# Optimization experiments

Hardware: AMD Instinct MI355X
Metric: run time of the kernel (lower is better)

Reference implementation:

```python
import jax, jax.numpy as jnp
import numpy as np

N_NODES = 100000
N_EDGES = 640000
C_IN = 128
C_OUT = 128
E_DIM = 64
LN_EPS = 1e-5


def setup_inputs() -> dict:
    key = jax.random.key(0)
    ks = jax.random.split(key, 10)
    x = jax.random.normal(ks[0], (N_NODES, C_IN), dtype=jnp.float32)
    edge_index = jax.random.randint(ks[1], (2, N_EDGES), 0, N_NODES, dtype=jnp.int32)
    edge_attr = jax.random.normal(ks[2], (N_EDGES, E_DIM), dtype=jnp.float32)
    # lin_edge: edge_dim -> in_channels
    We = jax.random.normal(ks[3], (E_DIM, C_IN), dtype=jnp.float32) / np.sqrt(E_DIM)
    be = jnp.zeros((C_IN,), dtype=jnp.float32)
    # mlp: Linear(C, 2C) -> LayerNorm(2C) -> ReLU -> Linear(2C, C_OUT)
    W1 = jax.random.normal(ks[4], (C_IN, 2 * C_IN), dtype=jnp.float32) / np.sqrt(C_IN)
    b1 = jnp.zeros((2 * C_IN,), dtype=jnp.float32)
    gamma = jnp.ones((2 * C_IN,), dtype=jnp.float32)
    beta = jnp.zeros((2 * C_IN,), dtype=jnp.float32)
    W2 = jax.random.normal(ks[5], (2 * C_IN, C_OUT), dtype=jnp.float32) / np.sqrt(2 * C_IN)
    b2 = jnp.zeros((C_OUT,), dtype=jnp.float32)
    eps = jnp.zeros((1,), dtype=jnp.float32)  # learnable GIN epsilon, init 0
    return {"x": x, "edge_index": edge_index, "edge_attr": edge_attr,
            "We": We, "be": be, "W1": W1, "b1": b1, "gamma": gamma,
            "beta": beta, "W2": W2, "b2": b2, "eps": eps}


def reference(x, edge_index, edge_attr, We, be, W1, b1, gamma, beta, W2, b2, eps):
    # edge feature projection: [E, E_DIM] @ [E_DIM, C] -> [E, C]
    real_edge_attr = edge_attr @ We + be
    # gather source-node features (edge_index[1]), add edge features, relu
    message = jax.nn.relu(x[edge_index[1]] + real_edge_attr)  # [E, C]
    # scatter-add to destination nodes (edge_index[0])
    message_reduce = jax.ops.segment_sum(message, edge_index[0], num_segments=x.shape[0])
    h = (1.0 + eps) * x + message_reduce  # [N, C]
    # MLP: Linear -> LayerNorm -> ReLU -> Linear
    h1 = h @ W1 + b1  # [N, 2C]
    mu = jnp.mean(h1, axis=-1, keepdims=True)
    var = jnp.mean(jnp.square(h1 - mu), axis=-1, keepdims=True)
    h1 = (h1 - mu) * jax.lax.rsqrt(var + LN_EPS) * gamma + beta
    h1 = jax.nn.relu(h1)
    return h1 @ W2 + b2  # [N, C_OUT]
```

## Files before the change

### kernel.cpp

```cpp
#include <hip/hip_runtime.h>
#include <hip/hip_bf16.h>
#include <stdint.h>

#define NNODES 100000
#define NEDGES 640000
#define CIN 128
#define EDIM 64
#define C2 256
#define LN_EPS 1e-5f
#define NW 6144
#define PP 105
#define NB 391

typedef __attribute__((ext_vector_type(8))) short bf16x8;
typedef __attribute__((ext_vector_type(4))) float f32x4;
typedef __attribute__((ext_vector_type(4))) uint32_t u32x4;
typedef __attribute__((ext_vector_type(4))) int i32x4;

__device__ __forceinline__ ushort f2bf(float f) {
    uint32_t u = __float_as_uint(f);
    uint32_t r = (u + 0x7fffu + ((u >> 16) & 1u)) >> 16;
    return (ushort)r;
}
__device__ __forceinline__ ushort f2bf_u(uint32_t u) {
    return (ushort)((u + 0x7fffu + ((u >> 16) & 1u)) >> 16);
}
__device__ __forceinline__ uint32_t pack2(float a, float b) {
    return (uint32_t)f2bf(a) | ((uint32_t)f2bf(b) << 16);
}
__device__ __forceinline__ float bf2f_lo(uint32_t u) { return __uint_as_float(u << 16); }
__device__ __forceinline__ float bf2f_hi(uint32_t u) { return __uint_as_float(u & 0xffff0000u); }

union U16 { uint4 u; bf16x8 v; };

__global__ __launch_bounds__(256) void k_prep(
    const float* __restrict__ x, const float* __restrict__ W1,
    const float* __restrict__ W2, uint32_t* __restrict__ xbf,
    ushort* __restrict__ W1T, ushort* __restrict__ W2T,
    int* __restrict__ cursor)
{
    const int bid = blockIdx.x;
    if (bid < 6250) {
        const int i = bid * 256 + threadIdx.x;
        const float4* xg = (const float4*)x;
        const float4 v0 = xg[i * 2];
        const float4 v1 = xg[i * 2 + 1];
        uint4 o;
        o.x = pack2(v0.x, v0.y); o.y = pack2(v0.z, v0.w);
        o.z = pack2(v1.x, v1.y); o.w = pack2(v1.z, v1.w);
        ((uint4*)xbf)[i] = o;
    } else if (bid < 6506) {
        const int idx = (bid - 6250) * 256 + threadIdx.x;
        if (idx < 32768) {
            const int k = idx >> 8, c = idx & 255;
            W1T[c * 128 + k] = f2bf(W1[idx]);
        } else {
            const int j = idx - 32768;
            const int k = j >> 7, c = j & 127;
            W2T[c * 256 + k] = f2bf(W2[j]);
        }
    } else {
        const int n = (bid - 6506) * 256 + threadIdx.x;
        if (n < NNODES) cursor[n] = 0;
    }
}

__global__ __launch_bounds__(256) void k_hist(const int* __restrict__ ei,
                                              int* __restrict__ counts)
{
    const int e = blockIdx.x * 256 + threadIdx.x;
    atomicAdd(&counts[ei[e]], 1);
}

__global__ __launch_bounds__(256) void k_sA(const int* __restrict__ counts,
                                            int* __restrict__ bsum)
{
    const int t = threadIdx.x, lane = t & 63, wv = t >> 6;
    const int i = blockIdx.x * 256 + t;
    int s = (i < NNODES) ? counts[i] : 0;
#pragma unroll
    for (int off = 1; off < 64; off <<= 1) s += __shfl_xor(s, off);
    __shared__ int ws[4];
    if (lane == 0) ws[wv] = s;
    __syncthreads();
    if (t == 0) bsum[blockIdx.x] = ws[0] + ws[1] + ws[2] + ws[3];
}

__global__ __launch_bounds__(256) void k_sC(const int* __restrict__ bsum,
                                            int* __restrict__ cursor,
                                            int* __restrict__ rowptr)
{
    __shared__ int wred[4];
    __shared__ int ws[4];
    const int t = threadIdx.x, lane = t & 63, wv = t >> 6;

    int part = 0;
    for (int j = t; j < blockIdx.x; j += 256) part += bsum[j];
#pragma unroll
    for (int off = 1; off < 64; off <<= 1) part += __shfl_xor(part, off);
    if (lane == 0) wred[wv] = part;
    __syncthreads();
    const int blockoff = wred[0] + wred[1] + wred[2] + wred[3];

    const int i = blockIdx.x * 256 + t;
    const int v = (i < NNODES) ? cursor[i] : 0;
    int s = v;
#pragma unroll
    for (int off = 1; off < 64; off <<= 1) {
        const int u = __shfl_up(s, off);
        if (lane >= off) s += u;
    }
    if (lane == 63) ws[wv] = s;
    __syncthreads();
    int off0 = blockoff;
    for (int w = 0; w < wv; ++w) off0 += ws[w];
    const int excl = off0 + s - v;
    if (i < NNODES) { rowptr[i] = excl; cursor[i] = excl; }
    if (i == NNODES - 1) rowptr[NNODES] = excl + v;
}

__global__ __launch_bounds__(256) void k_fillp(const int* __restrict__ ei,
                                               int* __restrict__ cursor,
                                               int4* __restrict__ efs,
                                               const int* __restrict__ rowptr,
                                               int* __restrict__ naw,
                                               uint32_t* __restrict__ hbf)
{
    const int bid = blockIdx.x;
    if (bid < 2500) {
        const int e = bid * 256 + threadIdx.x;
        const int d = ei[e];
        const int pos = atomicAdd(&cursor[d], 1);
        int4 rec; rec.x = e; rec.y = ei[NEDGES + e]; rec.z = d; rec.w = 0;
        efs[pos] = rec;
    } else if (bid < 2525) {
        const int w = (bid - 2500) * 256 + threadIdx.x;
        if (w > NW) return;
        if (w == NW) { naw[w] = NNODES; return; }
        const int target = min(w * PP, NEDGES);
        int lo = 0, hi = NNODES;
        while (lo < hi) {
            const int mid = (lo + hi) >> 1;
            if (rowptr[mid] < target) lo = mid + 1; else hi = mid;
        }
        naw[w] = lo;
    } else {
        const int n = (bid - 2525) * 256 + threadIdx.x;
        if (n < NNODES && rowptr[n] == rowptr[n + 1]) {
            uint32_t* r = hbf + (size_t)n * 64;
#pragma unroll
            for (int i = 0; i < 64; ++i) r[i] = 0;
        }
    }
}

__global__ __launch_bounds__(256, 3) void k_edge(
    const uint32_t* __restrict__ xbf, const float* __restrict__ ea,
    const float* __restrict__ We, const float* __restrict__ be,
    const int4* __restrict__ efs, const int* __restrict__ naw,
    const int* __restrict__ rowptr, uint32_t* __restrict__ hbf)
{
    __shared__ float msgl[4 * 16 * 128];
    const int tid = threadIdx.x;
    const int l = tid & 63, q = l >> 4, m16 = l & 15;
    const int wv = tid >> 6;
    const int w = blockIdx.x * 4 + wv;

    bf16x8 bfw[2][8];
#pragma unroll
    for (int ks = 0; ks < 2; ++ks)
#pragma unroll
        for (int t = 0; t < 8; ++t) {
            const int c = m16 + 16 * t;
#pragma unroll
            for (int j = 0; j < 8; ++j)
                bfw[ks][t][j] = (short)f2bf(We[(ks * 32 + q * 8 + j) * CIN + c]);
        }
    const float2 bev = ((const float2*)be)[l];

    const int n0 = naw[w], n1 = naw[w + 1];
    const int ps = rowptr[n0], pe = rowptr[n1];
    char* msb = (char*)msgl + wv * 8192;
    const int pmax = NEDGES - 1;

    int cur = -1;
    float a0 = 0.f, a1 = 0.f;

    for (int ts = ps; ts < pe; ts += 16) {
        const int nt = min(16, pe - ts);
        const int pp = min(ts + m16, pmax);
        const i32x4 rec = __builtin_nontemporal_load((const i32x4*)(efs + pp));
        const int ep = rec[0], sb = rec[1], db = rec[2];

        const u32x4* ar4 = (const u32x4*)(ea + (size_t)ep * EDIM + q * 8);
        const u32x4 uf0 = __builtin_nontemporal_load(ar4);
        const u32x4 uf1 = __builtin_nontemporal_load(ar4 + 1);
        const u32x4 ug0 = __builtin_nontemporal_load(ar4 + 8);
        const u32x4 ug1 = __builtin_nontemporal_load(ar4 + 9);

        uint xr[16];
#pragma unroll
        for (int jj = 0; jj < 16; ++jj) {
            const int sj = __builtin_amdgcn_readlane(sb, jj);
            if (jj < nt) xr[jj] = xbf[(size_t)sj * 64 + l];
        }

        bf16x8 A0, A1;
        A0[0] = (short)f2bf_u(uf0[0]); A0[1] = (short)f2bf_u(uf0[1]);
        A0[2] = (short)f2bf_u(uf0[2]); A0[3] = (short)f2bf_u(uf0[3]);
        A0[4] = (short)f2bf_u(uf1[0]); A0[5] = (short)f2bf_u(uf1[1]);
        A0[6] = (short)f2bf_u(uf1[2]); A0[7] = (short)f2bf_u(uf1[3]);
        A1[0] = (short)f2bf_u(ug0[0]); A1[1] = (short)f2bf_u(ug0[1]);
        A1[2] = (short)f2bf_u(ug0[2]); A1[3] = (short)f2bf_u(ug0[3]);
        A1[4] = (short)f2bf_u(ug1[0]); A1[5] = (short)f2bf_u(ug1[1]);
        A1[6] = (short)f2bf_u(ug1[2]); A1[7] = (short)f2bf_u(ug1[3]);

#pragma unroll
        for (int hf = 0; hf < 2; ++hf) {
            f32x4 acc4[4];
#pragma unroll
            for (int t4 = 0; t4 < 4; ++t4) acc4[t4] = (f32x4){0.f, 0.f, 0.f, 0.f};
#pragma unroll
            for (int t4 = 0; t4 < 4; ++t4) {
                acc4[t4] = __builtin_amdgcn_mfma_f32_16x16x32_bf16(A0, bfw[0][hf * 4 + t4], acc4[t4], 0, 0, 0);
                acc4[t4] = __builtin_amdgcn_mfma_f32_16x16x32_bf16(A1, bfw[1][hf * 4 + t4], acc4[t4], 0, 0, 0);
            }
#pragma unroll
            for (int t4 = 0; t4 < 4; ++t4) {
                const int col = m16 + 16 * (hf * 4 + t4);
#pragma unroll
                for (int r = 0; r < 4; ++r) {
                    const int row = q * 4 + r;
                    *(float*)(msb + row * 512 + ((4 * col) ^ ((row & 7) << 4))) = acc4[t4][r];
                }
            }
        }

#pragma unroll
        for (int jj = 0; jj < 16; ++jj) {
            if (jj < nt) {
                const int dj = __builtin_amdgcn_readlane(db, jj);
                if (dj != cur) {
                    if (cur >= 0)
                        __builtin_nontemporal_store(pack2(a0, a1),
                                                    hbf + (size_t)cur * 64 + l);
                    cur = dj; a0 = 0.f; a1 = 0.f;
                }
                const uint32_t xu = xr[jj];
                const float2 mv = *(const float2*)(msb + jj * 512 + ((8 * l) ^ ((jj & 7) << 4)));
                a0 += fmaxf(bf2f_lo(xu) + mv.x + bev.x, 0.f);
                a1 += fmaxf(bf2f_hi(xu) + mv.y + bev.y, 0.f);
            }
        }
    }
    if (cur >= 0)
        __builtin_nontemporal_store(pack2(a0, a1), hbf + (size_t)cur * 64 + l);
}

__global__ __launch_bounds__(512, 4) void k23_fused(
    const uint32_t* __restrict__ hbf, const uint32_t* __restrict__ xbf,
    const float* __restrict__ eps, const ushort* __restrict__ W1T,
    const ushort* __restrict__ W2T, const float* __restrict__ b1,
    const float* __restrict__ gamma, const float* __restrict__ beta,
    const float* __restrict__ b2, float* __restrict__ out)
{
    __shared__ ushort w1t[CIN * C2];

    const int tid = threadIdx.x;
    {
        const uint4* w1g = (const uint4*)W1T;
#pragma unroll
        for (int i = tid; i < 4096; i += 512) {
            const int c = i >> 4, inb = (i & 15) << 4;
            *(uint4*)((char*)w1t + c * 256 + (inb ^ ((c & 15) << 4))) = w1g[i];
        }
    }
    const float s1p = 1.0f + eps[0];
    __syncthreads();

    const int l = tid & 63, q = l >> 4, m16 = l & 15;
    const int w = tid >> 6;
    const int n0 = blockIdx.x * 128 + w * 16;
    const int rowA = min(n0 + m16, NNODES - 1);

    f32x4 acc[16];
#pragma unroll
    for (int t = 0; t < 16; ++t) acc[t] = (f32x4){0.f, 0.f, 0.f, 0.f};

    const char* w1b = (const char*)w1t;
#pragma unroll
    for (int ks = 0; ks < 4; ++ks) {
        const uint4 su = *(const uint4*)(hbf + (size_t)rowA * 64 + ks * 16 + q * 4);
        const uint4 xu = *(const uint4*)(xbf + (size_t)rowA * 64 + ks * 16 + q * 4);
        U16 A;
        A.v[0] = (short)f2bf(fmaf(s1p, bf2f_lo(xu.x), bf2f_lo(su.x)));
        A.v[1] = (short)f2bf(fmaf(s1p, bf2f_hi(xu.x), bf2f_hi(su.x)));
        A.v[2] = (short)f2bf(fmaf(s1p, bf2f_lo(xu.y), bf2f_lo(su.y)));
        A.v[3] = (short)f2bf(fmaf(s1p, bf2f_hi(xu.y), bf2f_hi(su.y)));
        A.v[4] = (short)f2bf(fmaf(s1p, bf2f_lo(xu.z), bf2f_lo(su.z)));
        A.v[5] = (short)f2bf(fmaf(s1p, bf2f_hi(xu.z), bf2f_hi(su.z)));
        A.v[6] = (short)f2bf(fmaf(s1p, bf2f_lo(xu.w), bf2f_lo(su.w)));
        A.v[7] = (short)f2bf(fmaf(s1p, bf2f_hi(xu.w), bf2f_hi(su.w)));
        const int inrow = (ks * 64 + q * 16) ^ (m16 << 4);
#pragma unroll
        for (int t = 0; t < 16; ++t) {
            U16 B; B.u = *(const uint4*)(w1b + (size_t)(m16 + 16 * t) * 256 + inrow);
            acc[t] = __builtin_amdgcn_mfma_f32_16x16x32_bf16(A.v, B.v, acc[t], 0, 0, 0);
        }
    }

    float s[4] = {0.f, 0.f, 0.f, 0.f}, sq[4] = {0.f, 0.f, 0.f, 0.f};
#pragma unroll
    for (int t = 0; t < 16; ++t) {
        const float bb = b1[m16 + 16 * t];
#pragma unroll
        for (int r = 0; r < 4; ++r) {
            acc[t][r] += bb;
            s[r]  += acc[t][r];
            sq[r] += acc[t][r] * acc[t][r];
        }
    }
#pragma unroll
    for (int off = 1; off < 16; off <<= 1)
#pragma unroll
        for (int r = 0; r < 4; ++r) {
            s[r]  += __shfl_xor(s[r],  off);
            sq[r] += __shfl_xor(sq[r], off);
        }
    float mu[4], is[4];
#pragma unroll
    for (int r = 0; r < 4; ++r) {
        mu[r] = s[r] * (1.0f / 256.0f);
        const float var = sq[r] * (1.0f / 256.0f) - mu[r] * mu[r];
        is[r] = rsqrtf(var + LN_EPS);
    }

    __syncthreads();

    char* hls = (char*)w1t + w * 8192;
#pragma unroll
    for (int t = 0; t < 16; ++t) {
        const int c = m16 + 16 * t;
        const float g = gamma[c], b = beta[c];
#pragma unroll
        for (int r = 0; r < 4; ++r) {
            const int row = q * 4 + r;
            const float o = fmaxf((acc[t][r] - mu[r]) * is[r] * g + b, 0.0f);
            *(ushort*)(hls + row * 512 + ((2 * c) ^ (row << 4))) = f2bf(o);
        }
    }
    __syncthreads();

    f32x4 acc2[8];
#pragma unroll
    for (int t = 0; t < 8; ++t) acc2[t] = (f32x4){0.f, 0.f, 0.f, 0.f};

    const char* w2g = (const char*)W2T;
#pragma unroll
    for (int ks = 0; ks < 8; ++ks) {
        const int inrow = (ks * 64 + q * 16) ^ (m16 << 4);
        const int inrow2 = ks * 64 + q * 16;
        U16 A; A.u = *(const uint4*)(hls + m16 * 512 + inrow);
#pragma unroll
        for (int t = 0; t < 8; ++t) {
            U16 B; B.u = *(const uint4*)(w2g + (size_t)(m16 + 16 * t) * 512 + inrow2);
            acc2[t] = __builtin_amdgcn_mfma_f32_16x16x32_bf16(A.v, B.v, acc2[t], 0, 0, 0);
        }
    }
#pragma unroll
    for (int t = 0; t < 8; ++t) {
        const int c = m16 + 16 * t;
        const float bb = b2[c];
#pragma unroll
        for (int r = 0; r < 4; ++r) {
            const int row = n0 + q * 4 + r;
            if (row < NNODES)
                out[(size_t)row * CIN + c] = acc2[t][r] + bb;
        }
    }
}

extern "C" void kernel_launch(void* const* d_in, const int* in_sizes, int n_in,
                              void* d_out, int out_size, void* d_ws, size_t ws_size,
                              hipStream_t stream)
{
    const float* x     = (const float*)d_in[0];
    const int*   ei    = (const int*)d_in[1];
    const float* ea    = (const float*)d_in[2];
    const float* We    = (const float*)d_in[3];
    const float* be    = (const float*)d_in[4];
    const float* W1    = (const float*)d_in[5];
    const float* b1    = (const float*)d_in[6];
    const float* gamma = (const float*)d_in[7];
    const float* beta  = (const float*)d_in[8];
    const float* W2    = (const float*)d_in[9];
    const float* b2    = (const float*)d_in[10];
    const float* eps   = (const float*)d_in[11];

    char* wsB = (char*)d_ws;
    uint32_t* hbf   = (uint32_t*)wsB;
    int*      rowptr= (int*)(wsB + 25600000);
    int*      cursor= (int*)(wsB + 26001408);
    int4*     efs   = (int4*)(wsB + 26401408);
    int*      naw   = (int*)(wsB + 36641408);
    int*      bsum  = (int*)(wsB + 36666368);
    uint32_t* xbf   = (uint32_t*)(wsB + 36668416);
    ushort*   W1T   = (ushort*)(wsB + 62268416);
    ushort*   W2T   = (ushort*)(wsB + 62333952);

    k_prep <<<6897, 256, 0, stream>>>(x, W1, W2, xbf, W1T, W2T, cursor);
    k_hist <<<NEDGES / 256, 256, 0, stream>>>(ei, cursor);
    k_sA   <<<NB, 256, 0, stream>>>(cursor, bsum);
    k_sC   <<<NB, 256, 0, stream>>>(bsum, cursor, rowptr);
    k_fillp<<<2916, 256, 0, stream>>>(ei, cursor, efs, rowptr, naw, hbf);

    k_edge <<<NW / 4, 256, 0, stream>>>(xbf, ea, We, be, efs, naw,
                                        rowptr, hbf);

    k23_fused<<<(NNODES + 127) / 128, 512, 0, stream>>>(hbf, xbf, eps, W1T, W2T,
                                                        b1, gamma, beta, b2,
                                                        (float*)d_out);
}
```

Before: 262.9 us.

## Read W1 directly from global memory in fused MLP and shrink blocks

The fused MLP kernel stops staging the full W1 matrix in shared memory. It reads B fragments straight from global memory, where the small weight matrix should stay cache-resident. Blocks shrink to 256 threads covering 64 nodes, and each wave keeps its own shared-memory slice for the hidden activations, so the block-wide barriers are removed. The edge kernel also changes its nontemporal stores of the aggregated h to normal stores, so they stay in cache for the next kernel. The trade-off is that W1 fragment loads now go through L1/L2 instead of LDS, which may raise latency in the first GEMM.

```diff
diff --git a/kernel.cpp b/kernel.cpp
--- a/kernel.cpp
+++ b/kernel.cpp
@@ -242,8 +242,7 @@
                 const int dj = __builtin_amdgcn_readlane(db, jj);
                 if (dj != cur) {
                     if (cur >= 0)
-                        __builtin_nontemporal_store(pack2(a0, a1),
-                                                    hbf + (size_t)cur * 64 + l);
+                        hbf[(size_t)cur * 64 + l] = pack2(a0, a1);
                     cur = dj; a0 = 0.f; a1 = 0.f;
                 }
                 const uint32_t xu = xr[jj];
@@ -254,40 +253,30 @@
         }
     }
     if (cur >= 0)
-        __builtin_nontemporal_store(pack2(a0, a1), hbf + (size_t)cur * 64 + l);
-}
-
-__global__ __launch_bounds__(512, 4) void k23_fused(
+        hbf[(size_t)cur * 64 + l] = pack2(a0, a1);
+}
+
+__global__ __launch_bounds__(256, 4) void k23_fused(
     const uint32_t* __restrict__ hbf, const uint32_t* __restrict__ xbf,
     const float* __restrict__ eps, const ushort* __restrict__ W1T,
     const ushort* __restrict__ W2T, const float* __restrict__ b1,
     const float* __restrict__ gamma, const float* __restrict__ beta,
     const float* __restrict__ b2, float* __restrict__ out)
 {
-    __shared__ ushort w1t[CIN * C2];
+    __shared__ ushort h1t[4 * 4096];
 
     const int tid = threadIdx.x;
-    {
-        const uint4* w1g = (const uint4*)W1T;
-#pragma unroll
-        for (int i = tid; i < 4096; i += 512) {
-            const int c = i >> 4, inb = (i & 15) << 4;
-            *(uint4*)((char*)w1t + c * 256 + (inb ^ ((c & 15) << 4))) = w1g[i];
-        }
-    }
+    const int l = tid & 63, q = l >> 4, m16 = l & 15;
+    const int wv = tid >> 6;
+    const int n0 = blockIdx.x * 64 + wv * 16;
+    const int rowA = min(n0 + m16, NNODES - 1);
     const float s1p = 1.0f + eps[0];
-    __syncthreads();
-
-    const int l = tid & 63, q = l >> 4, m16 = l & 15;
-    const int w = tid >> 6;
-    const int n0 = blockIdx.x * 128 + w * 16;
-    const int rowA = min(n0 + m16, NNODES - 1);
 
     f32x4 acc[16];
 #pragma unroll
     for (int t = 0; t < 16; ++t) acc[t] = (f32x4){0.f, 0.f, 0.f, 0.f};
 
-    const char* w1b = (const char*)w1t;
+    const char* w1g = (const char*)W1T;
 #pragma unroll
     for (int ks = 0; ks < 4; ++ks) {
         const uint4 su = *(const uint4*)(hbf + (size_t)rowA * 64 + ks * 16 + q * 4);
@@ -301,10 +290,10 @@
         A.v[5] = (short)f2bf(fmaf(s1p, bf2f_hi(xu.z), bf2f_hi(su.z)));
         A.v[6] = (short)f2bf(fmaf(s1p, bf2f_lo(xu.w), bf2f_lo(su.w)));
         A.v[7] = (short)f2bf(fmaf(s1p, bf2f_hi(xu.w), bf2f_hi(su.w)));
-        const int inrow = (ks * 64 + q * 16) ^ (m16 << 4);
+        const int inrow = ks * 64 + q * 16;
 #pragma unroll
         for (int t = 0; t < 16; ++t) {
-            U16 B; B.u = *(const uint4*)(w1b + (size_t)(m16 + 16 * t) * 256 + inrow);
+            U16 B; B.u = *(const uint4*)(w1g + (size_t)(m16 + 16 * t) * 256 + inrow);
             acc[t] = __builtin_amdgcn_mfma_f32_16x16x32_bf16(A.v, B.v, acc[t], 0, 0, 0);
         }
     }
@@ -335,9 +324,7 @@
         is[r] = rsqrtf(var + LN_EPS);
     }
 
-    __syncthreads();
-
-    char* hls = (char*)w1t + w * 8192;
+    char* hls = (char*)h1t + wv * 8192;
 #pragma unroll
     for (int t = 0; t < 16; ++t) {
         const int c = m16 + 16 * t;
@@ -349,7 +336,6 @@
             *(ushort*)(hls + row * 512 + ((2 * c) ^ (row << 4))) = f2bf(o);
         }
     }
-    __syncthreads();
 
     f32x4 acc2[8];
 #pragma unroll
@@ -417,7 +403,7 @@
     k_edge <<<NW / 4, 256, 0, stream>>>(xbf, ea, We, be, efs, naw,
                                         rowptr, hbf);
 
-    k23_fused<<<(NNODES + 127) / 128, 512, 0, stream>>>(hbf, xbf, eps, W1T, W2T,
-                                                        b1, gamma, beta, b2,
-                                                        (float*)d_out);
-}
+    k23_fused<<<(NNODES + 63) / 64, 256, 0, stream>>>(hbf, xbf, eps, W1T, W2T,
+                                                      b1, gamma, beta, b2,
+                                                      (float*)d_out);
+}
```

Result: slower. 297.4 us (+13.1%).
